# Optimization experiments

Hardware: AMD Instinct MI355X
Metric: run time of the kernel (lower is better)

Reference implementation:

```python
import jax, jax.numpy as jnp
import numpy as np

TEMPERATURE = 0.5
NEG_FILL = -9000000000000000.0


def setup_inputs() -> dict:
    key = jax.random.key(0)
    k1, k2 = jax.random.split(key)
    z1 = jax.random.normal(k1, (4096, 256), dtype=jnp.float32)
    z2 = jax.random.normal(k2, (4096, 256), dtype=jnp.float32)
    return {"z1": z1, "z2": z2}


def reference(z1, z2):
    N = z1.shape[0]
    z = jnp.concatenate([z1, z2], axis=0)  # [2N, d]
    # cosine similarity: normalize once (eps matches torch's 1e-8) then GEMM
    norm = jnp.maximum(jnp.linalg.norm(z, axis=-1, keepdims=True), 1e-8)
    zn = z / norm
    sim = (zn @ zn.T) / TEMPERATURE  # [2N, 2N]
    # mask out self-similarity on the diagonal
    diag = jnp.eye(2 * N, dtype=bool)
    sim = jnp.where(diag, NEG_FILL, sim)
    labels = jnp.concatenate([jnp.arange(N) + N, jnp.arange(N)])  # positive pairs
    logp = jax.nn.log_softmax(sim, axis=-1)
    loss = -jnp.mean(jnp.take_along_axis(logp, labels[:, None], axis=1))
    return loss
```

## Files before the change

### kernel.cpp

```cpp
#include <hip/hip_runtime.h>
#include <hip/hip_bf16.h>


#define TWO_N 8192
#define NPAIR 4096
#define DDIM  256
#define NT    64
#define INV_T 2.0f

typedef __attribute__((ext_vector_type(8))) short bf16x8;
typedef __attribute__((ext_vector_type(4))) float f32x4;

typedef __attribute__((address_space(1))) void gvoid_t;
typedef __attribute__((address_space(3))) void lvoid_t;

__device__ __forceinline__ void gload_lds16(const void* g, void* l) {
    __builtin_amdgcn_global_load_lds((gvoid_t*)g, (lvoid_t*)l, 16, 0, 0);
}

__global__ void k_normalize(const float* __restrict__ z1,
                            const float* __restrict__ z2,
                            __hip_bfloat16* __restrict__ zn,
                            float* __restrict__ e_diag,
                            float* __restrict__ pos,
                            float* __restrict__ row_sumexp,
                            float* __restrict__ out) {
    if (threadIdx.x < 8) row_sumexp[blockIdx.x * 8 + threadIdx.x] = 0.0f;
    if (blockIdx.x == 0 && threadIdx.x == 0) out[0] = 0.0f;

    const int w    = threadIdx.x >> 6;
    const int lane = threadIdx.x & 63;
    const int i    = blockIdx.x * 4 + w;

    float4 a = ((const float4*)(z1 + (size_t)i * DDIM))[lane];
    float4 b = ((const float4*)(z2 + (size_t)i * DDIM))[lane];

    float s1 = a.x * a.x + a.y * a.y + a.z * a.z + a.w * a.w;
    float s2 = b.x * b.x + b.y * b.y + b.z * b.z + b.w * b.w;
    float dd = a.x * b.x + a.y * b.y + a.z * b.z + a.w * b.w;
#pragma unroll
    for (int m = 1; m < 64; m <<= 1) {
        s1 += __shfl_xor(s1, m, 64);
        s2 += __shfl_xor(s2, m, 64);
        dd += __shfl_xor(dd, m, 64);
    }

    float inv1 = 1.0f / fmaxf(sqrtf(s1), 1e-8f);
    float inv2 = 1.0f / fmaxf(sqrtf(s2), 1e-8f);

    __hip_bfloat16 q1[4], q2[4];
    q1[0] = __float2bfloat16(a.x * inv1); q1[1] = __float2bfloat16(a.y * inv1);
    q1[2] = __float2bfloat16(a.z * inv1); q1[3] = __float2bfloat16(a.w * inv1);
    q2[0] = __float2bfloat16(b.x * inv2); q2[1] = __float2bfloat16(b.y * inv2);
    q2[2] = __float2bfloat16(b.z * inv2); q2[3] = __float2bfloat16(b.w * inv2);

    float qs1 = 0.0f, qs2 = 0.0f;
#pragma unroll
    for (int j = 0; j < 4; ++j) {
        float f1 = __bfloat162float(q1[j]);
        float f2 = __bfloat162float(q2[j]);
        qs1 += f1 * f1;
        qs2 += f2 * f2;
    }
#pragma unroll
    for (int m = 1; m < 64; m <<= 1) {
        qs1 += __shfl_xor(qs1, m, 64);
        qs2 += __shfl_xor(qs2, m, 64);
    }

    *reinterpret_cast<uint2*>(zn + (size_t)i * DDIM + lane * 4) =
        *reinterpret_cast<uint2*>(q1);
    *reinterpret_cast<uint2*>(zn + (size_t)(i + NPAIR) * DDIM + lane * 4) =
        *reinterpret_cast<uint2*>(q2);

    if (lane == 0) {
        e_diag[i]         = __expf(qs1 * INV_T);
        e_diag[i + NPAIR] = __expf(qs2 * INV_T);
        pos[i]            = dd * inv1 * inv2 * INV_T;
    }
}

__global__ __launch_bounds__(512, 2)
void k_gemm_rows(const __hip_bfloat16* __restrict__ zn,
                 float* __restrict__ row_sumexp) {
    __shared__ __align__(128) __hip_bfloat16 Asmem[128 * DDIM];

    const int tid  = threadIdx.x;
    const int lane = tid & 63;
    const int w    = tid >> 6;
    const int wr   = w >> 2;
    const int wc   = w & 3;
    const int lr   = lane & 15;
    const int quad = lane >> 4;

    const int panel    = blockIdx.x >> 3;
    const int chunk    = blockIdx.x & 7;
    const int row_base = panel * 128;

    {
        const int ck = (tid & 24) | ((tid & 7) ^ ((tid >> 5) & 7));
        const char* gA = (const char*)(zn + (size_t)row_base * DDIM)
                       + (tid >> 5) * (DDIM * 2) + ck * 16;
        char* lA = (char*)Asmem + tid * 16;
#pragma unroll
        for (int j = 0; j < 8; ++j)
            gload_lds16(gA + (size_t)j * 16 * (DDIM * 2), lA + j * 8192);
    }

    int pa[4];
#pragma unroll
    for (int mi = 0; mi < 4; ++mi)
        pa[mi] = (wr * 64 + mi * 16 + lr) * (DDIM * 2) + ((quad ^ (lr & 7)) << 4);

    f32x4 acc[4][2];
    float rs[4][4];
#pragma unroll
    for (int mi = 0; mi < 4; ++mi)
#pragma unroll
        for (int r = 0; r < 4; ++r) rs[mi][r] = 0.0f;

    auto epi_accum = [&]() {
#pragma unroll
        for (int mi = 0; mi < 4; ++mi)
#pragma unroll
            for (int r = 0; r < 4; ++r) {
                rs[mi][r] += __expf(acc[mi][0][r] * INV_T)
                           + __expf(acc[mi][1][r] * INV_T);
            }
    };

#pragma unroll 1
    for (int tt = 0; tt < 8; ++tt) {
        const int col_base = (chunk * 8 + tt) * 128;
        const __hip_bfloat16* gB0 =
            zn + (size_t)(col_base + wc * 32 + lr) * DDIM + quad * 8;

        bf16x8 Bfr[8][2];
#pragma unroll
        for (int ks = 0; ks < 8; ++ks) {
            const __hip_bfloat16* p0 = gB0 + ks * 32;
            const __hip_bfloat16* p1 = p0 + 16 * DDIM;
            asm volatile("global_load_dwordx4 %0, %1, off"
                         : "=v"(Bfr[ks][0]) : "v"(p0) : "memory");
            asm volatile("global_load_dwordx4 %0, %1, off"
                         : "=v"(Bfr[ks][1]) : "v"(p1) : "memory");
        }

        if (tt == 0) {
            asm volatile("s_waitcnt vmcnt(0)" ::: "memory");
            __syncthreads();
        } else {
            epi_accum();
            asm volatile("s_waitcnt vmcnt(0)" ::: "memory");
        }
        __builtin_amdgcn_sched_barrier(0);

#pragma unroll
        for (int mi = 0; mi < 4; ++mi)
#pragma unroll
            for (int ni = 0; ni < 2; ++ni)
                acc[mi][ni] = (f32x4){0.f, 0.f, 0.f, 0.f};

        bf16x8 afc[4];
#pragma unroll
        for (int mi = 0; mi < 4; ++mi)
            afc[mi] = *(const bf16x8*)((const char*)Asmem + pa[mi]);

#pragma unroll
        for (int kstep = 0; kstep < 8; ++kstep) {
            bf16x8 afn[4];
            if (kstep < 7) {
                const int kn   = kstep + 1;
                const int koff = (kn >> 1) << 7;
                const int kx   = (kn & 1) << 6;
#pragma unroll
                for (int mi = 0; mi < 4; ++mi)
                    afn[mi] = *(const bf16x8*)((const char*)Asmem + ((pa[mi] ^ kx) + koff));
            }
#pragma unroll
            for (int mi = 0; mi < 4; ++mi)
#pragma unroll
                for (int ni = 0; ni < 2; ++ni)
                    acc[mi][ni] = __builtin_amdgcn_mfma_f32_16x16x32_bf16(
                        afc[mi], Bfr[kstep][ni], acc[mi][ni], 0, 0, 0);
            if (kstep < 7) {
#pragma unroll
                for (int mi = 0; mi < 4; ++mi) afc[mi] = afn[mi];
            }
        }
    }

    epi_accum();

#pragma unroll
    for (int mi = 0; mi < 4; ++mi) {
#pragma unroll
        for (int r = 0; r < 4; ++r) {
            float v = rs[mi][r];
            v += __shfl_xor(v, 1, 64);
            v += __shfl_xor(v, 2, 64);
            v += __shfl_xor(v, 4, 64);
            v += __shfl_xor(v, 8, 64);
            if (lr == 0)
                atomicAdd(&row_sumexp[row_base + wr * 64 + mi * 16 + quad * 4 + r], v);
        }
    }
}

__global__ void k_final(const float* __restrict__ row_sumexp,
                        const float* __restrict__ e_diag,
                        const float* __restrict__ pos,
                        float* __restrict__ out) {
    const int i    = blockIdx.x * 256 + threadIdx.x;
    const int w    = threadIdx.x >> 6;
    const int lane = threadIdx.x & 63;

    float t = logf(row_sumexp[i] - e_diag[i])
            + logf(row_sumexp[i + NPAIR] - e_diag[i + NPAIR])
            - 2.0f * pos[i];
#pragma unroll
    for (int m = 1; m < 64; m <<= 1) t += __shfl_xor(t, m, 64);

    __shared__ float ps[4];
    if (lane == 0) ps[w] = t;
    __syncthreads();
    if (threadIdx.x == 0) {
        float s = (ps[0] + ps[1] + ps[2] + ps[3]) * (1.0f / (float)TWO_N);
        atomicAdd(out, s);
    }
}

extern "C" void kernel_launch(void* const* d_in, const int* in_sizes, int n_in,
                              void* d_out, int out_size, void* d_ws, size_t ws_size,
                              hipStream_t stream) {
    const float* z1 = (const float*)d_in[0];
    const float* z2 = (const float*)d_in[1];
    float* out = (float*)d_out;

    char* ws = (char*)d_ws;
    __hip_bfloat16* zn  = (__hip_bfloat16*)ws;
    float* row_sumexp   = (float*)(ws + (size_t)TWO_N * DDIM * 2);
    float* e_diag       = row_sumexp + TWO_N;
    float* pos          = e_diag + TWO_N;

    k_normalize<<<NPAIR / 4, 256, 0, stream>>>(z1, z2, zn, e_diag, pos,
                                               row_sumexp, out);
    k_gemm_rows<<<NT * 8, 512, 0, stream>>>(zn, row_sumexp);
    k_final<<<NPAIR / 256, 256, 0, stream>>>(row_sumexp, e_diag, pos, out);
}
```

Before: 132.9 us.

## Double-buffer B fragments in registers to overlap global loads with MFMA

Splits the B-operand register fragments into two buffers, A and B. The loads for the next column tile are issued before the MFMA k-loop runs on the current tile, and partial vmcnt waits let one tile's loads stay in flight during compute. Previously each tile waited for all of its loads before its MFMAs started. This doubles the VGPRs held for B, which could reduce occupancy or cause spills under launch_bounds(512,2).

```diff
diff --git a/kernel.cpp b/kernel.cpp
--- a/kernel.cpp
+++ b/kernel.cpp
@@ -112,12 +112,29 @@
     for (int mi = 0; mi < 4; ++mi)
         pa[mi] = (wr * 64 + mi * 16 + lr) * (DDIM * 2) + ((quad ^ (lr & 7)) << 4);
 
+    const __hip_bfloat16* gBw = zn + (size_t)(wc * 32 + lr) * DDIM + quad * 8;
+
     f32x4 acc[4][2];
     float rs[4][4];
 #pragma unroll
     for (int mi = 0; mi < 4; ++mi)
 #pragma unroll
         for (int r = 0; r < 4; ++r) rs[mi][r] = 0.0f;
+
+    bf16x8 BfrA[8][2], BfrB[8][2];
+
+    auto issueB = [&](bf16x8 (&B)[8][2], int tt) {
+        const __hip_bfloat16* gB0 = gBw + (size_t)(chunk * 8 + tt) * 128 * DDIM;
+#pragma unroll
+        for (int ks = 0; ks < 8; ++ks) {
+            const __hip_bfloat16* p0 = gB0 + ks * 32;
+            const __hip_bfloat16* p1 = p0 + 16 * DDIM;
+            asm volatile("global_load_dwordx4 %0, %1, off"
+                         : "=v"(B[ks][0]) : "v"(p0) : "memory");
+            asm volatile("global_load_dwordx4 %0, %1, off"
+                         : "=v"(B[ks][1]) : "v"(p1) : "memory");
+        }
+    };
 
     auto epi_accum = [&]() {
 #pragma unroll
@@ -129,43 +146,16 @@
             }
     };
 
-#pragma unroll 1
-    for (int tt = 0; tt < 8; ++tt) {
-        const int col_base = (chunk * 8 + tt) * 128;
-        const __hip_bfloat16* gB0 =
-            zn + (size_t)(col_base + wc * 32 + lr) * DDIM + quad * 8;
-
-        bf16x8 Bfr[8][2];
-#pragma unroll
-        for (int ks = 0; ks < 8; ++ks) {
-            const __hip_bfloat16* p0 = gB0 + ks * 32;
-            const __hip_bfloat16* p1 = p0 + 16 * DDIM;
-            asm volatile("global_load_dwordx4 %0, %1, off"
-                         : "=v"(Bfr[ks][0]) : "v"(p0) : "memory");
-            asm volatile("global_load_dwordx4 %0, %1, off"
-                         : "=v"(Bfr[ks][1]) : "v"(p1) : "memory");
-        }
-
-        if (tt == 0) {
-            asm volatile("s_waitcnt vmcnt(0)" ::: "memory");
-            __syncthreads();
-        } else {
-            epi_accum();
-            asm volatile("s_waitcnt vmcnt(0)" ::: "memory");
-        }
-        __builtin_amdgcn_sched_barrier(0);
-
+    auto kloop = [&](bf16x8 (&B)[8][2]) {
 #pragma unroll
         for (int mi = 0; mi < 4; ++mi)
 #pragma unroll
             for (int ni = 0; ni < 2; ++ni)
                 acc[mi][ni] = (f32x4){0.f, 0.f, 0.f, 0.f};
-
         bf16x8 afc[4];
 #pragma unroll
         for (int mi = 0; mi < 4; ++mi)
             afc[mi] = *(const bf16x8*)((const char*)Asmem + pa[mi]);
-
 #pragma unroll
         for (int kstep = 0; kstep < 8; ++kstep) {
             bf16x8 afn[4];
@@ -182,12 +172,38 @@
 #pragma unroll
                 for (int ni = 0; ni < 2; ++ni)
                     acc[mi][ni] = __builtin_amdgcn_mfma_f32_16x16x32_bf16(
-                        afc[mi], Bfr[kstep][ni], acc[mi][ni], 0, 0, 0);
+                        afc[mi], B[kstep][ni], acc[mi][ni], 0, 0, 0);
             if (kstep < 7) {
 #pragma unroll
                 for (int mi = 0; mi < 4; ++mi) afc[mi] = afn[mi];
             }
         }
+    };
+
+    issueB(BfrA, 0);
+    asm volatile("s_waitcnt vmcnt(0)" ::: "memory");
+    __syncthreads();
+    __builtin_amdgcn_sched_barrier(0);
+
+#pragma unroll 1
+    for (int p = 0; p < 4; ++p) {
+        const int te = 2 * p;
+
+        issueB(BfrB, te + 1);
+        if (p > 0) epi_accum();
+        asm volatile("s_waitcnt vmcnt(16)" ::: "memory");
+        __builtin_amdgcn_sched_barrier(0);
+        kloop(BfrA);
+
+        if (te + 2 < 8) issueB(BfrA, te + 2);
+        epi_accum();
+        if (te + 2 < 8) {
+            asm volatile("s_waitcnt vmcnt(16)" ::: "memory");
+        } else {
+            asm volatile("s_waitcnt vmcnt(0)" ::: "memory");
+        }
+        __builtin_amdgcn_sched_barrier(0);
+        kloop(BfrB);
     }
 
     epi_accum();
```

Measured after the change: 132.9 us. About the same (+0.1%).
